# Performance work log

Hardware: AMD Instinct MI355X
Metric: run time of the kernel (lower is better)

The kernel has to match this reference:

```python
import jax, jax.numpy as jnp
import numpy as np

B, N, D, H, L = 4, 256, 512, 8, 3
HD = D // H
K_SPARSE = max(1, int(N * 0.1))  # top-k edges per node
EPS = 1e-5  # torch LayerNorm default


def _mha(x, Wqkv, bqkv, Wo, bo):
    b, n, d = x.shape
    qkv = x @ Wqkv + bqkv
    q, k, v = jnp.split(qkv, 3, axis=-1)
    rs = lambda t: t.reshape(b, n, H, HD).transpose(0, 2, 1, 3)
    q, k, v = rs(q), rs(k), rs(v)
    att = jax.nn.softmax(jnp.einsum('bhqd,bhkd->bhqk', q, k) * (HD ** -0.5), axis=-1)
    out = jnp.einsum('bhqk,bhkd->bhqd', att, v).transpose(0, 2, 1, 3).reshape(b, n, d)
    return out @ Wo + bo


def _ln(x, g, b):
    m = x.mean(-1, keepdims=True)
    v = ((x - m) ** 2).mean(-1, keepdims=True)
    return (x - m) / jnp.sqrt(v + EPS) * g + b


def setup_inputs() -> dict:
    key = jax.random.key(0)
    ks = iter(jax.random.split(key, 32))
    rn = lambda *s: jax.random.normal(next(ks), s, jnp.float32) * 0.02
    return {
        'x': jax.random.normal(next(ks), (B, N, D), jnp.float32),
        'adjacency': jax.random.uniform(next(ks), (B, N, N), jnp.float32),
        'Wqkv': rn(L, D, 3 * D), 'bqkv': rn(L, 3 * D),
        'Wo': rn(L, D, D), 'bo': rn(L, D),
        'Wp1': rn(L - 1, D, D // 2), 'bp1': rn(L - 1, D // 2),
        'Wp2': rn(L - 1, D // 2, D), 'bp2': rn(L - 1, D),
        'Wfuse': rn(L * D, D), 'bfuse': rn(D),
        'ln_g': jnp.ones((D,), jnp.float32), 'ln_b': jnp.zeros((D,), jnp.float32),
        'We1': rn(2 * D, D), 'be1': rn(D), 'We2': rn(D, 1), 'be2': rn(1),
        'Ws_qkv': rn(D, 3 * D), 'bs_qkv': rn(3 * D),
        'Ws_o': rn(D, D), 'bs_o': rn(D),
    }


def reference(x, adjacency, Wqkv, bqkv, Wo, bo, Wp1, bp1, Wp2, bp2, Wfuse, bfuse,
              ln_g, ln_b, We1, be1, We2, be2, Ws_qkv, bs_qkv, Ws_o, bs_o):
    # --- HierarchicalGraphAttention ---
    cur = x
    level_outs = []
    for l in range(L):  # fixed small hierarchy loop
        a = _mha(cur, Wqkv[l], bqkv[l], Wo[l], bo[l])
        level_outs.append(a)
        if l < L - 1:
            p = jax.nn.relu(a @ Wp1[l] + bp1[l]) @ Wp2[l] + bp2[l]
            cur = p.reshape(B, -1, 2, D).mean(axis=2)  # pairwise pooling halves nodes
    # upsample each level back to N nodes (repeat_interleave), fuse
    fused = [jnp.repeat(o, N // o.shape[1], axis=1) for o in level_outs]
    hier = _ln(jax.nn.relu(jnp.concatenate(fused, axis=-1) @ Wfuse + bfuse), ln_g, ln_b)

    # --- SparseGraphOperations: O(N^2) edge scoring + per-row top-k ---
    # cat([x_i, x_j]) @ We1 == x_i @ We1[:D] + x_j @ We1[D:]
    hi = hier @ We1[:D]                      # [B,N,D]
    hj = hier @ We1[D:] + be1                # [B,N,D]
    pre = hi[:, :, None, :] + hj[:, None, :, :]  # [B,N,N,D]
    scores = jax.nn.sigmoid((jax.nn.relu(pre) @ We2 + be2)[..., 0])  # [B,N,N]
    scores = jnp.where(jnp.eye(N, dtype=bool)[None], 0.0, scores)    # i != j only
    _, idx = jax.lax.top_k(scores, K_SPARSE)  # [B,N,K]
    sparse_adj = jnp.zeros((B, N, N), jnp.float32).at[
        jnp.arange(B)[:, None, None], jnp.arange(N)[None, :, None], idx].set(1.0)

    attended = _mha(hier, Ws_qkv, bs_qkv, Ws_o, bs_o)
    return attended, sparse_adj
```

## Files before the change

### kernel.cpp

```cpp
#include <hip/hip_runtime.h>
#include <math.h>


typedef __attribute__((ext_vector_type(8))) short bf16x8;
typedef __attribute__((ext_vector_type(4))) float f32x4;
typedef __attribute__((ext_vector_type(8))) unsigned short ushort8v;

__device__ __forceinline__ unsigned short f2bf(float x) {
    union { float f; unsigned int u; } c; c.f = x;
    unsigned int r = (c.u + 0x7fffu + ((c.u >> 16) & 1u)) >> 16;
    return (unsigned short)r;
}

template <int TM>
__global__ __launch_bounds__(256) void gemm_v6(
    const float* __restrict__ A, const float* __restrict__ W,
    const float* __restrict__ bias, float* __restrict__ C,
    int M, int N, int K, int flags, int wmode)
{
    constexpr int RT = TM / 16;
    __shared__ float As[16][TM + 4];
    __shared__ float Ws[16][68];

    const int tid = threadIdx.x;
    const int tx = tid & 15, ty = tid >> 4;
    const int bm = blockIdx.y * TM, bn = blockIdx.x * 64;

    const float* Wp = W;
    const float* bp = bias;
    int wn = N, wcol = bn;
    if (wmode == 1) {
        int seg = (bm >= 1536) ? 2 : (bm >= 1024) ? 1 : 0;
        Wp += (size_t)seg * 262144;
    } else if (wmode == 2) {
        if (bn >= 512) Wp += 262144; else bp = nullptr;
        wn = 512; wcol = bn & 511;
    }

    constexpr int AV = (TM == 64) ? 4 : 2;
    const int ar = (TM == 64) ? (tid >> 2) : (tid >> 3);
    const int ac = (TM == 64) ? ((tid & 3) << 2) : ((tid & 7) << 1);
    const int wr = tid >> 4;
    const int wc = (tid & 15) << 2;

    const float* Aptr = A + (size_t)(bm + ar) * K + ac;
    const float* Wptr = Wp + (size_t)wr * wn + wcol + wc;

    float acc[RT][4] = {};
    float ra[AV], rw[4];

#define LOADREGS(k0_) do {                                                   \
        const float* ap_ = Aptr + (k0_);                                     \
        if constexpr (TM == 64) {                                            \
            float4 v_ = *(const float4*)ap_;                                 \
            ra[0]=v_.x; ra[1]=v_.y; ra[2]=v_.z; ra[3]=v_.w;                  \
        } else {                                                             \
            float2 v_ = *(const float2*)ap_; ra[0]=v_.x; ra[1]=v_.y;         \
        }                                                                    \
        float4 w_ = *(const float4*)(Wptr + (size_t)(k0_) * wn);             \
        rw[0]=w_.x; rw[1]=w_.y; rw[2]=w_.z; rw[3]=w_.w; } while (0)

    LOADREGS(0);

    for (int k0 = 0; k0 < K; k0 += 16) {
        if (k0) __syncthreads();
        #pragma unroll
        for (int u = 0; u < AV; ++u) As[ac + u][ar] = ra[u];
        #pragma unroll
        for (int u = 0; u < 4; ++u) Ws[wr][wc + u] = rw[u];
        __syncthreads();

        if (k0 + 16 < K) LOADREGS(k0 + 16);

        #pragma unroll
        for (int kk = 0; kk < 16; ++kk) {
            float a[RT];
            if constexpr (RT == 4) {
                float4 t = *(const float4*)&As[kk][ty * 4];
                a[0]=t.x; a[1]=t.y; a[2]=t.z; a[3]=t.w;
            } else {
                float2 t = *(const float2*)&As[kk][ty * 2];
                a[0]=t.x; a[1]=t.y;
            }
            float4 tw = *(const float4*)&Ws[kk][tx * 4];
            float w[4] = {tw.x, tw.y, tw.z, tw.w};
            #pragma unroll
            for (int i = 0; i < RT; ++i)
                #pragma unroll
                for (int j = 0; j < 4; ++j)
                    acc[i][j] = fmaf(a[i], w[j], acc[i][j]);
        }
    }
#undef LOADREGS

    #pragma unroll
    for (int j = 0; j < 4; ++j) {
        const int cn = bn + tx * 4 + j;
        const float bv = bp ? bp[wcol + tx * 4 + j] : 0.f;
        if (flags & 2) {
            #pragma unroll
            for (int pi = 0; pi < RT / 2; ++pi) {
                float f0 = acc[2 * pi][j] + bv;
                float f1 = acc[2 * pi + 1][j] + bv;
                if (flags & 1) { f0 = fmaxf(f0, 0.f); f1 = fmaxf(f1, 0.f); }
                int prow = ((bm + ty * RT) >> 1) + pi;
                C[(size_t)prow * N + cn] = (f0 + f1) * 0.5f;
            }
        } else {
            #pragma unroll
            for (int i = 0; i < RT; ++i) {
                float f = acc[i][j] + bv;
                if (flags & 1) f = fmaxf(f, 0.f);
                C[(size_t)(bm + ty * RT + i) * N + cn] = f;
            }
        }
    }
}

__global__ __launch_bounds__(256) void cvtT_kernel(
    const float* __restrict__ W, unsigned short* __restrict__ Wt, int K, int N)
{
    __shared__ unsigned short t[64][72];
    const int n0 = blockIdx.x * 64, k0 = blockIdx.y * 64;
    const int tid = threadIdx.x;
    const int rr = tid >> 4, c4 = (tid & 15) << 2;
    #pragma unroll
    for (int u = 0; u < 4; ++u) {
        const float4 v = *(const float4*)(W + (size_t)(k0 + rr + u * 16) * N + n0 + c4);
        t[c4 + 0][rr + u * 16] = f2bf(v.x);
        t[c4 + 1][rr + u * 16] = f2bf(v.y);
        t[c4 + 2][rr + u * 16] = f2bf(v.z);
        t[c4 + 3][rr + u * 16] = f2bf(v.w);
    }
    __syncthreads();
    const int orow = tid >> 2, oc = (tid & 3) << 4;
    unsigned short* dst = Wt + (size_t)(n0 + orow) * K + k0 + oc;
    *(ushort8v*)(dst + 0) = *(const ushort8v*)&t[orow][oc + 0];
    *(ushort8v*)(dst + 8) = *(const ushort8v*)&t[orow][oc + 8];
}

__global__ __launch_bounds__(256) void mfma_gemm(
    const unsigned short* __restrict__ Ab, const unsigned short* __restrict__ Bt,
    const float* __restrict__ bias, float* __restrict__ C,
    int M, int N, int K, int ldc)
{
    const int lane = threadIdx.x & 63;
    const int wv = threadIdx.x >> 6;
    const int bn = blockIdx.x * 64;
    const int bm = blockIdx.y * 128 + wv * 32;
    const int l15 = lane & 15;
    const int kb = (lane >> 4) * 8;

    const unsigned short* a0p = Ab + (size_t)(bm + l15) * K + kb;
    const unsigned short* a1p = a0p + (size_t)16 * K;
    const unsigned short* bp0 = Bt + (size_t)(bn + l15) * K + kb;

    f32x4 acc[2][4];
    #pragma unroll
    for (int i = 0; i < 2; ++i)
        #pragma unroll
        for (int j = 0; j < 4; ++j)
            acc[i][j] = (f32x4){0.f, 0.f, 0.f, 0.f};

    for (int k0 = 0; k0 < K; k0 += 32) {
        const bf16x8 a0 = *(const bf16x8*)(a0p + k0);
        const bf16x8 a1 = *(const bf16x8*)(a1p + k0);
        #pragma unroll
        for (int nf = 0; nf < 4; ++nf) {
            const bf16x8 b = *(const bf16x8*)(bp0 + (size_t)nf * 16 * K + k0);
            acc[0][nf] = __builtin_amdgcn_mfma_f32_16x16x32_bf16(a0, b, acc[0][nf], 0, 0, 0);
            acc[1][nf] = __builtin_amdgcn_mfma_f32_16x16x32_bf16(a1, b, acc[1][nf], 0, 0, 0);
        }
    }

    const int r0 = (lane >> 4) * 4;
    #pragma unroll
    for (int mf = 0; mf < 2; ++mf)
        #pragma unroll
        for (int nf = 0; nf < 4; ++nf) {
            const int col = bn + nf * 16 + l15;
            const float bv = bias ? bias[col] : 0.f;
            #pragma unroll
            for (int r = 0; r < 4; ++r) {
                const int row = bm + mf * 16 + r0 + r;
                C[(size_t)row * ldc + col] = acc[mf][nf][r] + bv;
            }
        }
}

template <int NT>
__global__ __launch_bounds__(256) void attn_v3(
    const float* __restrict__ qkv, float* __restrict__ out,
    unsigned short* __restrict__ outb, int n, int qstride)
{
    const int lane = threadIdx.x & 63;
    const int w    = threadIdx.x >> 6;
    const int h = blockIdx.y, b = blockIdx.z;
    const int q0 = blockIdx.x * 16;
    const size_t base = (size_t)b * n * qstride;

    __shared__ float q_lds[16][64];
    __shared__ float kv_lds[64][68];
    __shared__ float p_lds[16][256];

    {
        int r = threadIdx.x >> 4, c4 = (threadIdx.x & 15) << 2;
        float4 v = *(const float4*)(qkv + base + (size_t)(q0 + r) * qstride + h * 64 + c4);
        q_lds[r][c4 + 0] = v.x; q_lds[r][c4 + 1] = v.y;
        q_lds[r][c4 + 2] = v.z; q_lds[r][c4 + 3] = v.w;
    }

    const int r0 = w * 4;
    const int sr = threadIdx.x >> 2;
    const int sq = threadIdx.x & 3;

    float s[4][NT];

    #pragma unroll
    for (int t = 0; t < NT; ++t) {
        const int j0 = t * 64;
        __syncthreads();
        {
            const float* src = qkv + base + (size_t)(j0 + sr) * qstride + 512 + h * 64;
            #pragma unroll
            for (int u = 0; u < 4; ++u) {
                int c = u * 4 + sq;
                float4 v = *(const float4*)(src + c * 4);
                *(float4*)&kv_lds[sr][c * 4] = v;
            }
        }
        __syncthreads();
        float c0 = 0.f, c1 = 0.f, c2 = 0.f, c3 = 0.f;
        #pragma unroll
        for (int d = 0; d < 64; d += 4) {
            const float4 kv = *(const float4*)&kv_lds[lane][d];
            const float4 qa = *(const float4*)&q_lds[r0 + 0][d];
            const float4 qb = *(const float4*)&q_lds[r0 + 1][d];
            const float4 qc = *(const float4*)&q_lds[r0 + 2][d];
            const float4 qd = *(const float4*)&q_lds[r0 + 3][d];
            c0 = fmaf(qa.x, kv.x, c0); c0 = fmaf(qa.y, kv.y, c0);
            c0 = fmaf(qa.z, kv.z, c0); c0 = fmaf(qa.w, kv.w, c0);
            c1 = fmaf(qb.x, kv.x, c1); c1 = fmaf(qb.y, kv.y, c1);
            c1 = fmaf(qb.z, kv.z, c1); c1 = fmaf(qb.w, kv.w, c1);
            c2 = fmaf(qc.x, kv.x, c2); c2 = fmaf(qc.y, kv.y, c2);
            c2 = fmaf(qc.z, kv.z, c2); c2 = fmaf(qc.w, kv.w, c2);
            c3 = fmaf(qd.x, kv.x, c3); c3 = fmaf(qd.y, kv.y, c3);
            c3 = fmaf(qd.z, kv.z, c3); c3 = fmaf(qd.w, kv.w, c3);
        }
        s[0][t] = c0 * 0.125f; s[1][t] = c1 * 0.125f;
        s[2][t] = c2 * 0.125f; s[3][t] = c3 * 0.125f;
    }

    double inv[4];
    #pragma unroll
    for (int qr = 0; qr < 4; ++qr) {
        float m = s[qr][0];
        #pragma unroll
        for (int t = 1; t < NT; ++t) m = fmaxf(m, s[qr][t]);
        #pragma unroll
        for (int off = 32; off; off >>= 1) m = fmaxf(m, __shfl_xor(m, off));
        double sum = 0.0;
        #pragma unroll
        for (int t = 0; t < NT; ++t) {
            float p = expf(s[qr][t] - m);
            p_lds[r0 + qr][t * 64 + lane] = p;
            sum += (double)p;
        }
        #pragma unroll
        for (int off = 32; off; off >>= 1) sum += __shfl_xor(sum, off);
        inv[qr] = 1.0 / sum;
    }

    float o0 = 0.f, o1 = 0.f, o2 = 0.f, o3 = 0.f;
    #pragma unroll
    for (int t = 0; t < NT; ++t) {
        const int j0 = t * 64;
        __syncthreads();
        {
            const float* src = qkv + base + (size_t)(j0 + sr) * qstride + 1024 + h * 64;
            #pragma unroll
            for (int u = 0; u < 4; ++u) {
                int c = u * 4 + sq;
                float4 v = *(const float4*)(src + c * 4);
                kv_lds[c * 4 + 0][sr] = v.x;
                kv_lds[c * 4 + 1][sr] = v.y;
                kv_lds[c * 4 + 2][sr] = v.z;
                kv_lds[c * 4 + 3][sr] = v.w;
            }
        }
        __syncthreads();
        #pragma unroll
        for (int jl = 0; jl < 64; jl += 4) {
            const float4 vv = *(const float4*)&kv_lds[lane][jl];
            const float4 pa = *(const float4*)&p_lds[r0 + 0][t * 64 + jl];
            const float4 pb = *(const float4*)&p_lds[r0 + 1][t * 64 + jl];
            const float4 pc = *(const float4*)&p_lds[r0 + 2][t * 64 + jl];
            const float4 pd = *(const float4*)&p_lds[r0 + 3][t * 64 + jl];
            o0 = fmaf(pa.x, vv.x, o0); o0 = fmaf(pa.y, vv.y, o0);
            o0 = fmaf(pa.z, vv.z, o0); o0 = fmaf(pa.w, vv.w, o0);
            o1 = fmaf(pb.x, vv.x, o1); o1 = fmaf(pb.y, vv.y, o1);
            o1 = fmaf(pb.z, vv.z, o1); o1 = fmaf(pb.w, vv.w, o1);
            o2 = fmaf(pc.x, vv.x, o2); o2 = fmaf(pc.y, vv.y, o2);
            o2 = fmaf(pc.z, vv.z, o2); o2 = fmaf(pc.w, vv.w, o2);
            o3 = fmaf(pd.x, vv.x, o3); o3 = fmaf(pd.y, vv.y, o3);
            o3 = fmaf(pd.z, vv.z, o3); o3 = fmaf(pd.w, vv.w, o3);
        }
    }
    const size_t obase = ((size_t)(b * n + q0 + r0)) * 512 + h * 64 + lane;
    const float r0v = (float)((double)o0 * inv[0]);
    const float r1v = (float)((double)o1 * inv[1]);
    const float r2v = (float)((double)o2 * inv[2]);
    const float r3v = (float)((double)o3 * inv[3]);
    out[obase + 0 * 512] = r0v;
    out[obase + 1 * 512] = r1v;
    out[obase + 2 * 512] = r2v;
    out[obase + 3 * 512] = r3v;
    if (outb) {
        outb[obase + 0 * 512] = f2bf(r0v);
        outb[obase + 1 * 512] = f2bf(r1v);
        outb[obase + 2 * 512] = f2bf(r2v);
        outb[obase + 3 * 512] = f2bf(r3v);
    }
}

__global__ __launch_bounds__(64) void ln3_kernel(
    const float* __restrict__ y, const float* __restrict__ bf,
    const float* __restrict__ g, const float* __restrict__ bta,
    float* __restrict__ out, unsigned short* __restrict__ outb)
{
    const int r = blockIdx.x, lane = threadIdx.x;
    const int b = r >> 8, i = r & 255;
    const float* y0 = y + (size_t)r * 512;
    const float* y1 = y + (size_t)(1024 + b * 128 + (i >> 1)) * 512;
    const float* y2 = y + (size_t)(1536 + b * 64 + (i >> 2)) * 512;
    double v[8];
    double sum = 0.0;
    #pragma unroll
    for (int t = 0; t < 8; ++t) {
        int d = t * 64 + lane;
        double s = (double)y0[d] + (double)y1[d] + (double)y2[d] + (double)bf[d];
        s = s > 0.0 ? s : 0.0;
        v[t] = s; sum += s;
    }
    #pragma unroll
    for (int off = 32; off; off >>= 1) sum += __shfl_xor(sum, off);
    const double mean = sum * (1.0 / 512.0);
    double ss = 0.0;
    #pragma unroll
    for (int t = 0; t < 8; ++t) { double d = v[t] - mean; ss += d * d; }
    #pragma unroll
    for (int off = 32; off; off >>= 1) ss += __shfl_xor(ss, off);
    const double rstd = 1.0 / sqrt(ss * (1.0 / 512.0) + 1e-5);
    #pragma unroll
    for (int t = 0; t < 8; ++t) {
        int d = t * 64 + lane;
        float f = (float)((v[t] - mean) * rstd * (double)g[d] + (double)bta[d]);
        out[(size_t)r * 512 + d] = f;
        outb[(size_t)r * 512 + d] = f2bf(f);
    }
}

__global__ __launch_bounds__(256) void scores_v4(
    const float* __restrict__ hq, int stride, int off,
    const float* __restrict__ We2, const float* __restrict__ be2,
    float* __restrict__ S)
{
    __shared__ float Hi[128][34];
    __shared__ float Hj[128][34];
    const int b = blockIdx.z;
    const int i0 = blockIdx.y * 32, j0 = blockIdx.x * 32;
    const int tid = threadIdx.x;
    const int tx = tid & 15, ty = tid >> 4;

    const int si = tid >> 3;
    const int sd = (tid & 7) << 2;

    const float* hip = hq + (size_t)(b * 256 + i0 + si) * stride + off + sd;
    const float* hjp = hq + (size_t)(b * 256 + j0 + si) * stride + off + 512 + sd;

    double a00 = 0.0, a01 = 0.0, a10 = 0.0, a11 = 0.0;

    for (int k0 = 0; k0 < 512; k0 += 128) {
        __syncthreads();
        #pragma unroll
        for (int u = 0; u < 4; ++u) {
            const int dch = u * 32 + sd;
            float4 v = *(const float4*)(hip + k0 + u * 32);
            Hi[dch + 0][si] = v.x; Hi[dch + 1][si] = v.y;
            Hi[dch + 2][si] = v.z; Hi[dch + 3][si] = v.w;
            float4 w = *(const float4*)(hjp + k0 + u * 32);
            Hj[dch + 0][si] = w.x; Hj[dch + 1][si] = w.y;
            Hj[dch + 2][si] = w.z; Hj[dch + 3][si] = w.w;
        }
        __syncthreads();
        #pragma unroll 16
        for (int kk = 0; kk < 128; ++kk) {
            const double wv = (double)We2[k0 + kk];
            const float2 hi = *(const float2*)&Hi[kk][ty * 2];
            const float2 hj = *(const float2*)&Hj[kk][tx * 2];
            a00 += (double)fmaxf(hi.x + hj.x, 0.f) * wv;
            a01 += (double)fmaxf(hi.x + hj.y, 0.f) * wv;
            a10 += (double)fmaxf(hi.y + hj.x, 0.f) * wv;
            a11 += (double)fmaxf(hi.y + hj.y, 0.f) * wv;
        }
    }

    const double bb = (double)be2[0];
    const int gi0 = i0 + ty * 2, gj0 = j0 + tx * 2;
    double zz[2][2] = {{a00, a01}, {a10, a11}};
    #pragma unroll
    for (int ii = 0; ii < 2; ++ii)
        #pragma unroll
        for (int jj = 0; jj < 2; ++jj) {
            double z = zz[ii][jj] + bb;
            float sc_ = (float)(1.0 / (1.0 + exp(-z)));
            if (gi0 + ii == gj0 + jj) sc_ = 0.f;
            S[(size_t)(b * 256 + gi0 + ii) * 256 + gj0 + jj] = sc_;
        }
}

__global__ __launch_bounds__(64) void topk_kernel(
    const float* __restrict__ S, float* __restrict__ out)
{
    const int row = blockIdx.x;
    const int lane = threadIdx.x;
    float v[4]; int sel[4] = {0, 0, 0, 0};
    #pragma unroll
    for (int t = 0; t < 4; ++t) v[t] = S[(size_t)row * 256 + t * 64 + lane];
    for (int it = 0; it < 25; ++it) {
        float bv = v[0]; int bi = lane;
        #pragma unroll
        for (int t = 1; t < 4; ++t) {
            int idx = t * 64 + lane;
            if (v[t] > bv) { bv = v[t]; bi = idx; }
        }
        #pragma unroll
        for (int off = 32; off; off >>= 1) {
            float ov = __shfl_xor(bv, off);
            int   oi = __shfl_xor(bi, off);
            if (ov > bv || (ov == bv && oi < bi)) { bv = ov; bi = oi; }
        }
        if ((bi & 63) == lane) { int t = bi >> 6; sel[t] = 1; v[t] = -INFINITY; }
    }
    #pragma unroll
    for (int t = 0; t < 4; ++t)
        out[(size_t)row * 256 + t * 64 + lane] = (float)sel[t];
}

extern "C" void kernel_launch(void* const* d_in, const int* in_sizes, int n_in,
                              void* d_out, int out_size, void* d_ws, size_t ws_size,
                              hipStream_t stream)
{
    const float* x      = (const float*)d_in[0];
    const float* Wqkv   = (const float*)d_in[2];
    const float* bqkv   = (const float*)d_in[3];
    const float* Wo     = (const float*)d_in[4];
    const float* bo     = (const float*)d_in[5];
    const float* Wp1    = (const float*)d_in[6];
    const float* bp1    = (const float*)d_in[7];
    const float* Wp2    = (const float*)d_in[8];
    const float* bp2    = (const float*)d_in[9];
    const float* Wfuse  = (const float*)d_in[10];
    const float* bfuse  = (const float*)d_in[11];
    const float* ln_g   = (const float*)d_in[12];
    const float* ln_b   = (const float*)d_in[13];
    const float* We1    = (const float*)d_in[14];
    const float* be1    = (const float*)d_in[15];
    const float* We2    = (const float*)d_in[16];
    const float* be2    = (const float*)d_in[17];
    const float* Ws_qkv = (const float*)d_in[18];
    const float* bs_qkv = (const float*)d_in[19];
    const float* Ws_o   = (const float*)d_in[20];
    const float* bs_o   = (const float*)d_in[21];

    float* out_att    = (float*)d_out;
    float* out_sparse = out_att + 4 * 256 * 512;

    float* ws    = (float*)d_ws;
    float* qkvb  = ws;
    float* attnb = qkvb + 1572864;
    float* lvls  = attnb + 524288;
    float* poolb = lvls + 917504;
    float* curb  = poolb + 131072;
    float* hier  = curb + 262144;
    float* scb   = hier + 524288;
    float* hibjb = scb + 262144;
    float* bfp   = hibjb + 1048576;
    unsigned short* hier_b  = (unsigned short*)bfp;
    unsigned short* attnb_b = hier_b + 524288;
    unsigned short* wqkvT   = attnb_b + 524288;
    unsigned short* wsoT    = wqkvT + 786432;

    float* lvl0 = lvls;
    float* lvl1 = lvls + 1024 * 512;
    float* lvl2 = lvls + 1536 * 512;

    auto G64 = [&](const float* A, const float* W, const float* bias, float* C,
                   int M, int N, int K, int flags, int wmode) {
        gemm_v6<64><<<dim3(N / 64, M / 64), 256, 0, stream>>>(
            A, W, bias, C, M, N, K, flags, wmode);
    };
    auto G32 = [&](const float* A, const float* W, const float* bias, float* C,
                   int M, int N, int K, int flags, int wmode) {
        gemm_v6<32><<<dim3(N / 64, M / 32), 256, 0, stream>>>(
            A, W, bias, C, M, N, K, flags, wmode);
    };

    cvtT_kernel<<<dim3(1536 / 64, 512 / 64), 256, 0, stream>>>(Ws_qkv, wqkvT, 512, 1536);
    cvtT_kernel<<<dim3(512 / 64, 512 / 64), 256, 0, stream>>>(Ws_o, wsoT, 512, 512);

    G64(x, Wqkv, bqkv, qkvb, 1024, 1536, 512, 0, 0);
    attn_v3<4><<<dim3(16, 8, 4), 256, 0, stream>>>(qkvb, attnb, nullptr, 256, 1536);
    G32(attnb, Wo, bo, lvl0, 1024, 512, 512, 0, 0);
    G32(lvl0, Wp1, bp1, poolb, 1024, 256, 512, 3, 0);
    G32(poolb, Wp2, bp2, curb, 512, 512, 256, 0, 0);

    G64(curb, Wqkv + 512 * 1536, bqkv + 1536, qkvb, 512, 1536, 512, 0, 0);
    attn_v3<2><<<dim3(8, 8, 4), 256, 0, stream>>>(qkvb, attnb, nullptr, 128, 1536);
    G32(attnb, Wo + 512 * 512, bo + 512, lvl1, 512, 512, 512, 0, 0);
    G32(lvl1, Wp1 + 512 * 256, bp1 + 256, poolb, 512, 256, 512, 3, 0);
    G32(poolb, Wp2 + 256 * 512, bp2 + 512, curb, 256, 512, 256, 0, 0);

    G32(curb, Wqkv + 2 * 512 * 1536, bqkv + 2 * 1536, qkvb, 256, 1536, 512, 0, 0);
    attn_v3<1><<<dim3(4, 8, 4), 256, 0, stream>>>(qkvb, attnb, nullptr, 64, 1536);
    G32(attnb, Wo + 2 * 512 * 512, bo + 2 * 512, lvl2, 256, 512, 512, 0, 0);

    G64(lvls, Wfuse, nullptr, qkvb, 1792, 512, 512, 0, 1);
    ln3_kernel<<<1024, 64, 0, stream>>>(qkvb, bfuse, ln_g, ln_b, hier, hier_b);

    G64(hier, We1, be1, hibjb, 1024, 1024, 512, 0, 2);
    scores_v4<<<dim3(8, 8, 4), 256, 0, stream>>>(hibjb, 1024, 0, We2, be2, scb);
    topk_kernel<<<1024, 64, 0, stream>>>(scb, out_sparse);

    mfma_gemm<<<dim3(1536 / 64, 1024 / 128), 256, 0, stream>>>(
        hier_b, wqkvT, bs_qkv, qkvb, 1024, 1536, 512, 1536);
    attn_v3<4><<<dim3(16, 8, 4), 256, 0, stream>>>(qkvb, attnb, attnb_b, 256, 1536);
    mfma_gemm<<<dim3(512 / 64, 1024 / 128), 256, 0, stream>>>(
        attnb_b, wsoT, bs_o, out_att, 1024, 512, 512, 512);
}
```

Before: 383.9 us.

## Pack independent kernels into combined launches and split the fuse GEMM per level

Kernel bodies become device functions on shared scratch memory, and independent stages share one launch by dispatching on block index. The weight conversions run with the first QKV GEMM, each Wp1 GEMM with its level's Wfuse slice, We1 with the final QKV MFMA GEMM, final attention with edge scoring, and top-k with the output projection. The fuse GEMM is split into three per-level GEMMs that reuse the hibjb buffer as scratch, and the layer-norm now packs four rows per block. The aim is fewer launches and better GPU fill from small grids; the cost is larger shared-memory footprints and the mixed-work blocks may finish unevenly.

```diff
diff --git a/kernel.cpp b/kernel.cpp
--- a/kernel.cpp
+++ b/kernel.cpp
@@ -13,26 +13,23 @@
 }
 
 template <int TM>
-__global__ __launch_bounds__(256) void gemm_v6(
-    const float* __restrict__ A, const float* __restrict__ W,
+__device__ __forceinline__ void gemm_dev(
+    char* smem, const float* __restrict__ A, const float* __restrict__ W,
     const float* __restrict__ bias, float* __restrict__ C,
-    int M, int N, int K, int flags, int wmode)
+    int M, int N, int K, int flags, int wmode, int bx, int by)
 {
     constexpr int RT = TM / 16;
-    __shared__ float As[16][TM + 4];
-    __shared__ float Ws[16][68];
+    float (*As)[TM + 4] = (float (*)[TM + 4])smem;
+    float (*Ws)[68] = (float (*)[68])(smem + 16 * (TM + 4) * sizeof(float));
 
     const int tid = threadIdx.x;
     const int tx = tid & 15, ty = tid >> 4;
-    const int bm = blockIdx.y * TM, bn = blockIdx.x * 64;
+    const int bm = by * TM, bn = bx * 64;
 
     const float* Wp = W;
     const float* bp = bias;
     int wn = N, wcol = bn;
-    if (wmode == 1) {
-        int seg = (bm >= 1536) ? 2 : (bm >= 1024) ? 1 : 0;
-        Wp += (size_t)seg * 262144;
-    } else if (wmode == 2) {
+    if (wmode == 2) {
         if (bn >= 512) Wp += 262144; else bp = nullptr;
         wn = 512; wcol = bn & 511;
     }
@@ -117,11 +114,23 @@
     }
 }
 
-__global__ __launch_bounds__(256) void cvtT_kernel(
-    const float* __restrict__ W, unsigned short* __restrict__ Wt, int K, int N)
-{
-    __shared__ unsigned short t[64][72];
-    const int n0 = blockIdx.x * 64, k0 = blockIdx.y * 64;
+template <int TM>
+__global__ __launch_bounds__(256) void gemm_v6(
+    const float* __restrict__ A, const float* __restrict__ W,
+    const float* __restrict__ bias, float* __restrict__ C,
+    int M, int N, int K, int flags, int wmode)
+{
+    constexpr int SB = (TM == 64) ? 8704 : 6656;
+    __shared__ __align__(16) char smem[SB];
+    gemm_dev<TM>(smem, A, W, bias, C, M, N, K, flags, wmode, blockIdx.x, blockIdx.y);
+}
+
+__device__ __forceinline__ void cvt_dev(
+    char* smem, const float* __restrict__ W, unsigned short* __restrict__ Wt,
+    int K, int N, int bx, int by)
+{
+    unsigned short (*t)[72] = (unsigned short (*)[72])smem;
+    const int n0 = bx * 64, k0 = by * 64;
     const int tid = threadIdx.x;
     const int rr = tid >> 4, c4 = (tid & 15) << 2;
     #pragma unroll
@@ -139,15 +148,15 @@
     *(ushort8v*)(dst + 8) = *(const ushort8v*)&t[orow][oc + 8];
 }
 
-__global__ __launch_bounds__(256) void mfma_gemm(
+__device__ __forceinline__ void mfma_dev(
     const unsigned short* __restrict__ Ab, const unsigned short* __restrict__ Bt,
     const float* __restrict__ bias, float* __restrict__ C,
-    int M, int N, int K, int ldc)
+    int M, int N, int K, int ldc, int bx, int by)
 {
     const int lane = threadIdx.x & 63;
     const int wv = threadIdx.x >> 6;
-    const int bn = blockIdx.x * 64;
-    const int bm = blockIdx.y * 128 + wv * 32;
+    const int bn = bx * 64;
+    const int bm = by * 128 + wv * 32;
     const int l15 = lane & 15;
     const int kb = (lane >> 4) * 8;
 
@@ -189,19 +198,20 @@
 }
 
 template <int NT>
-__global__ __launch_bounds__(256) void attn_v3(
-    const float* __restrict__ qkv, float* __restrict__ out,
-    unsigned short* __restrict__ outb, int n, int qstride)
-{
+__device__ __forceinline__ void attn_dev(
+    char* smem, const float* __restrict__ qkv, float* __restrict__ out,
+    unsigned short* __restrict__ outb, int n, int qstride,
+    int bx, int by, int bz)
+{
+    float (*q_lds)[64]  = (float (*)[64])smem;
+    float (*kv_lds)[68] = (float (*)[68])(smem + 4096);
+    float (*p_lds)[256] = (float (*)[256])(smem + 4096 + 17408);
+
     const int lane = threadIdx.x & 63;
     const int w    = threadIdx.x >> 6;
-    const int h = blockIdx.y, b = blockIdx.z;
-    const int q0 = blockIdx.x * 16;
+    const int h = by, b = bz;
+    const int q0 = bx * 16;
     const size_t base = (size_t)b * n * qstride;
-
-    __shared__ float q_lds[16][64];
-    __shared__ float kv_lds[64][68];
-    __shared__ float p_lds[16][256];
 
     {
         int r = threadIdx.x >> 4, c4 = (threadIdx.x & 15) << 2;
@@ -323,52 +333,24 @@
     }
 }
 
-__global__ __launch_bounds__(64) void ln3_kernel(
-    const float* __restrict__ y, const float* __restrict__ bf,
-    const float* __restrict__ g, const float* __restrict__ bta,
-    float* __restrict__ out, unsigned short* __restrict__ outb)
-{
-    const int r = blockIdx.x, lane = threadIdx.x;
-    const int b = r >> 8, i = r & 255;
-    const float* y0 = y + (size_t)r * 512;
-    const float* y1 = y + (size_t)(1024 + b * 128 + (i >> 1)) * 512;
-    const float* y2 = y + (size_t)(1536 + b * 64 + (i >> 2)) * 512;
-    double v[8];
-    double sum = 0.0;
-    #pragma unroll
-    for (int t = 0; t < 8; ++t) {
-        int d = t * 64 + lane;
-        double s = (double)y0[d] + (double)y1[d] + (double)y2[d] + (double)bf[d];
-        s = s > 0.0 ? s : 0.0;
-        v[t] = s; sum += s;
-    }
-    #pragma unroll
-    for (int off = 32; off; off >>= 1) sum += __shfl_xor(sum, off);
-    const double mean = sum * (1.0 / 512.0);
-    double ss = 0.0;
-    #pragma unroll
-    for (int t = 0; t < 8; ++t) { double d = v[t] - mean; ss += d * d; }
-    #pragma unroll
-    for (int off = 32; off; off >>= 1) ss += __shfl_xor(ss, off);
-    const double rstd = 1.0 / sqrt(ss * (1.0 / 512.0) + 1e-5);
-    #pragma unroll
-    for (int t = 0; t < 8; ++t) {
-        int d = t * 64 + lane;
-        float f = (float)((v[t] - mean) * rstd * (double)g[d] + (double)bta[d]);
-        out[(size_t)r * 512 + d] = f;
-        outb[(size_t)r * 512 + d] = f2bf(f);
-    }
-}
-
-__global__ __launch_bounds__(256) void scores_v4(
-    const float* __restrict__ hq, int stride, int off,
+template <int NT>
+__global__ __launch_bounds__(256) void attn_v3(
+    const float* __restrict__ qkv, float* __restrict__ out,
+    unsigned short* __restrict__ outb, int n, int qstride)
+{
+    __shared__ __align__(16) char smem[37888];
+    attn_dev<NT>(smem, qkv, out, outb, n, qstride, blockIdx.x, blockIdx.y, blockIdx.z);
+}
+
+__device__ __forceinline__ void scores_dev(
+    char* smem, const float* __restrict__ hq, int stride, int off,
     const float* __restrict__ We2, const float* __restrict__ be2,
-    float* __restrict__ S)
-{
-    __shared__ float Hi[128][34];
-    __shared__ float Hj[128][34];
-    const int b = blockIdx.z;
-    const int i0 = blockIdx.y * 32, j0 = blockIdx.x * 32;
+    float* __restrict__ S, int bx, int by, int bz)
+{
+    float (*Hi)[34] = (float (*)[34])smem;
+    float (*Hj)[34] = (float (*)[34])(smem + 17408);
+    const int b = bz;
+    const int i0 = by * 32, j0 = bx * 32;
     const int tid = threadIdx.x;
     const int tx = tid & 15, ty = tid >> 4;
 
@@ -419,11 +401,10 @@
         }
 }
 
-__global__ __launch_bounds__(64) void topk_kernel(
-    const float* __restrict__ S, float* __restrict__ out)
-{
-    const int row = blockIdx.x;
-    const int lane = threadIdx.x;
+__device__ __forceinline__ void topk_wave(
+    const float* __restrict__ S, float* __restrict__ out, int row)
+{
+    const int lane = threadIdx.x & 63;
     float v[4]; int sel[4] = {0, 0, 0, 0};
     #pragma unroll
     for (int t = 0; t < 4; ++t) v[t] = S[(size_t)row * 256 + t * 64 + lane];
@@ -445,6 +426,127 @@
     #pragma unroll
     for (int t = 0; t < 4; ++t)
         out[(size_t)row * 256 + t * 64 + lane] = (float)sel[t];
+}
+
+__global__ __launch_bounds__(256) void ln3_k(
+    const float* __restrict__ y, const float* __restrict__ bf,
+    const float* __restrict__ g, const float* __restrict__ bta,
+    float* __restrict__ out, unsigned short* __restrict__ outb)
+{
+    const int r = blockIdx.x * 4 + (threadIdx.x >> 6);
+    const int lane = threadIdx.x & 63;
+    const int b = r >> 8, i = r & 255;
+    const float* y0 = y + (size_t)r * 512;
+    const float* y1 = y + (size_t)(1024 + b * 128 + (i >> 1)) * 512;
+    const float* y2 = y + (size_t)(1536 + b * 64 + (i >> 2)) * 512;
+    double v[8];
+    double sum = 0.0;
+    #pragma unroll
+    for (int t = 0; t < 8; ++t) {
+        int d = t * 64 + lane;
+        double s = (double)y0[d] + (double)y1[d] + (double)y2[d] + (double)bf[d];
+        s = s > 0.0 ? s : 0.0;
+        v[t] = s; sum += s;
+    }
+    #pragma unroll
+    for (int off = 32; off; off >>= 1) sum += __shfl_xor(sum, off);
+    const double mean = sum * (1.0 / 512.0);
+    double ss = 0.0;
+    #pragma unroll
+    for (int t = 0; t < 8; ++t) { double d = v[t] - mean; ss += d * d; }
+    #pragma unroll
+    for (int off = 32; off; off >>= 1) ss += __shfl_xor(ss, off);
+    const double rstd = 1.0 / sqrt(ss * (1.0 / 512.0) + 1e-5);
+    #pragma unroll
+    for (int t = 0; t < 8; ++t) {
+        int d = t * 64 + lane;
+        float f = (float)((v[t] - mean) * rstd * (double)g[d] + (double)bta[d]);
+        out[(size_t)r * 512 + d] = f;
+        outb[(size_t)r * 512 + d] = f2bf(f);
+    }
+}
+
+__global__ __launch_bounds__(256) void pack_qkv_cvt(
+    const float* x, const float* Wqkv, const float* bqkv, float* qkvb,
+    const float* Wsqkv, unsigned short* wqkvT,
+    const float* Wso, unsigned short* wsoT)
+{
+    __shared__ __align__(16) char smem[9216];
+    const int bid = blockIdx.x;
+    if (bid < 384) {
+        gemm_dev<64>(smem, x, Wqkv, bqkv, qkvb, 1024, 1536, 512, 0, 0,
+                     bid % 24, bid / 24);
+    } else if (bid < 576) {
+        const int r = bid - 384;
+        cvt_dev(smem, Wsqkv, wqkvT, 512, 1536, r % 24, r / 24);
+    } else {
+        const int r = bid - 576;
+        cvt_dev(smem, Wso, wsoT, 512, 512, r % 8, r / 8);
+    }
+}
+
+__global__ __launch_bounds__(256) void pack_wp1_fuse(
+    const float* lvl, const float* Wp1, const float* bp1, float* poolb,
+    const float* Wfseg, float* ydst, int Mw, int Mf, int nb_w)
+{
+    __shared__ __align__(16) char smem[8704];
+    const int bid = blockIdx.x;
+    if (bid < nb_w) {
+        gemm_dev<32>(smem, lvl, Wp1, bp1, poolb, Mw, 256, 512, 3, 0,
+                     bid % 4, bid / 4);
+    } else {
+        const int r = bid - nb_w;
+        gemm_dev<64>(smem, lvl, Wfseg, nullptr, ydst, Mf, 512, 512, 0, 0,
+                     r % 8, r / 8);
+    }
+}
+
+__global__ __launch_bounds__(256) void pack_we1_mfma(
+    const float* hier, const float* We1, const float* be1, float* hibjb,
+    const unsigned short* hier_b, const unsigned short* wqkvT,
+    const float* bs_qkv, float* qkvb)
+{
+    __shared__ __align__(16) char smem[8704];
+    const int bid = blockIdx.x;
+    if (bid < 256) {
+        gemm_dev<64>(smem, hier, We1, be1, hibjb, 1024, 1024, 512, 0, 2,
+                     bid % 16, bid / 16);
+    } else {
+        const int r = bid - 256;
+        mfma_dev(hier_b, wqkvT, bs_qkv, qkvb, 1024, 1536, 512, 1536,
+                 r % 24, r / 24);
+    }
+}
+
+__global__ __launch_bounds__(256) void pack_attnF_scores(
+    const float* qkvb, float* attnb, unsigned short* attnb_b,
+    const float* hibjb, const float* We2, const float* be2, float* scb)
+{
+    __shared__ __align__(16) char smem[37888];
+    const int bid = blockIdx.x;
+    if (bid < 512) {
+        attn_dev<4>(smem, qkvb, attnb, attnb_b, 256, 1536,
+                    bid % 16, (bid / 16) % 8, bid / 128);
+    } else {
+        const int r = bid - 512;
+        scores_dev(smem, hibjb, 1024, 0, We2, be2, scb,
+                   r % 8, (r / 8) % 8, r / 64);
+    }
+}
+
+__global__ __launch_bounds__(256) void pack_topk_mfma(
+    const float* scb, float* out_sparse,
+    const unsigned short* attnb_b, const unsigned short* wsoT,
+    const float* bs_o, float* out_att)
+{
+    const int bid = blockIdx.x;
+    if (bid < 256) {
+        topk_wave(scb, out_sparse, bid * 4 + (threadIdx.x >> 6));
+    } else {
+        const int r = bid - 256;
+        mfma_dev(attnb_b, wsoT, bs_o, out_att, 1024, 512, 512, 512,
+                 r % 8, r / 8);
+    }
 }
 
 extern "C" void kernel_launch(void* const* d_in, const int* in_sizes, int n_in,
@@ -485,8 +587,8 @@
     float* hier  = curb + 262144;
     float* scb   = hier + 524288;
     float* hibjb = scb + 262144;
-    float* bfp   = hibjb + 1048576;
-    unsigned short* hier_b  = (unsigned short*)bfp;
+    float* ybuf  = hibjb;
+    unsigned short* hier_b  = (unsigned short*)(hibjb + 1048576);
     unsigned short* attnb_b = hier_b + 524288;
     unsigned short* wqkvT   = attnb_b + 524288;
     unsigned short* wsoT    = wqkvT + 786432;
@@ -506,35 +608,33 @@
             A, W, bias, C, M, N, K, flags, wmode);
     };
 
-    cvtT_kernel<<<dim3(1536 / 64, 512 / 64), 256, 0, stream>>>(Ws_qkv, wqkvT, 512, 1536);
-    cvtT_kernel<<<dim3(512 / 64, 512 / 64), 256, 0, stream>>>(Ws_o, wsoT, 512, 512);
-
-    G64(x, Wqkv, bqkv, qkvb, 1024, 1536, 512, 0, 0);
+    pack_qkv_cvt<<<640, 256, 0, stream>>>(x, Wqkv, bqkv, qkvb,
+                                          Ws_qkv, wqkvT, Ws_o, wsoT);
     attn_v3<4><<<dim3(16, 8, 4), 256, 0, stream>>>(qkvb, attnb, nullptr, 256, 1536);
     G32(attnb, Wo, bo, lvl0, 1024, 512, 512, 0, 0);
-    G32(lvl0, Wp1, bp1, poolb, 1024, 256, 512, 3, 0);
+    pack_wp1_fuse<<<256, 256, 0, stream>>>(lvl0, Wp1, bp1, poolb,
+                                           Wfuse, ybuf, 1024, 1024, 128);
     G32(poolb, Wp2, bp2, curb, 512, 512, 256, 0, 0);
 
     G64(curb, Wqkv + 512 * 1536, bqkv + 1536, qkvb, 512, 1536, 512, 0, 0);
     attn_v3<2><<<dim3(8, 8, 4), 256, 0, stream>>>(qkvb, attnb, nullptr, 128, 1536);
     G32(attnb, Wo + 512 * 512, bo + 512, lvl1, 512, 512, 512, 0, 0);
-    G32(lvl1, Wp1 + 512 * 256, bp1 + 256, poolb, 512, 256, 512, 3, 0);
+    pack_wp1_fuse<<<128, 256, 0, stream>>>(lvl1, Wp1 + 512 * 256, bp1 + 256, poolb,
+                                           Wfuse + 262144, ybuf + 1024 * 512,
+                                           512, 512, 64);
     G32(poolb, Wp2 + 256 * 512, bp2 + 512, curb, 256, 512, 256, 0, 0);
 
     G32(curb, Wqkv + 2 * 512 * 1536, bqkv + 2 * 1536, qkvb, 256, 1536, 512, 0, 0);
     attn_v3<1><<<dim3(4, 8, 4), 256, 0, stream>>>(qkvb, attnb, nullptr, 64, 1536);
     G32(attnb, Wo + 2 * 512 * 512, bo + 2 * 512, lvl2, 256, 512, 512, 0, 0);
-
-    G64(lvls, Wfuse, nullptr, qkvb, 1792, 512, 512, 0, 1);
-    ln3_kernel<<<1024, 64, 0, stream>>>(qkvb, bfuse, ln_g, ln_b, hier, hier_b);
-
-    G64(hier, We1, be1, hibjb, 1024, 1024, 512, 0, 2);
-    scores_v4<<<dim3(8, 8, 4), 256, 0, stream>>>(hibjb, 1024, 0, We2, be2, scb);
-    topk_kernel<<<1024, 64, 0, stream>>>(scb, out_sparse);
-
-    mfma_gemm<<<dim3(1536 / 64, 1024 / 128), 256, 0, stream>>>(
-        hier_b, wqkvT, bs_qkv, qkvb, 1024, 1536, 512, 1536);
-    attn_v3<4><<<dim3(16, 8, 4), 256, 0, stream>>>(qkvb, attnb, attnb_b, 256, 1536);
-    mfma_gemm<<<dim3(512 / 64, 1024 / 128), 256, 0, stream>>>(
-        attnb_b, wsoT, bs_o, out_att, 1024, 512, 512, 512);
-}
+    G64(lvl2, Wfuse + 524288, nullptr, ybuf + 1536 * 512, 256, 512, 512, 0, 0);
+
+    ln3_k<<<256, 256, 0, stream>>>(ybuf, bfuse, ln_g, ln_b, hier, hier_b);
+
+    pack_we1_mfma<<<448, 256, 0, stream>>>(hier, We1, be1, hibjb,
+                                           hier_b, wqkvT, bs_qkv, qkvb);
+    pack_attnF_scores<<<768, 256, 0, stream>>>(qkvb, attnb, attnb_b,
+                                               hibjb, We2, be2, scb);
+    pack_topk_mfma<<<320, 256, 0, stream>>>(scb, out_sparse,
+                                            attnb_b, wsoT, bs_o, out_att);
+}
```

Result: faster. 348.8 us, median of 2 (-9.1%).
